# Kernel tuning notes

Measured on AMD Instinct MI355X. Metric: run time of the kernel, lower is better.

## Reference

```python
import jax, jax.numpy as jnp
import numpy as np

B, T, C = 4, 1024, 768
E, K = 8, 2               # n_exp, top_k
N = B * T                 # num_tokens
# eval-mode capacity: floor(K * eval_capacity(2.0) * N / E), rounded even, >= min_capacity(4)
CAP = 2048


def setup_inputs() -> dict:
    key = jax.random.key(0)
    k0, k1, k2, k3 = jax.random.split(key, 4)
    s = 0.02
    return {
        "x": jax.random.normal(k0, (B, T, C), jnp.float32),
        "w_g": jax.random.normal(k1, (E, C), jnp.float32) * s,
        "c_fc": jax.random.normal(k2, (E, C, 4 * C), jnp.float32) * s,
        "fc_bias": jnp.zeros((E, 1, 4 * C), jnp.float32),
        "c_proj": jax.random.normal(k3, (E, 4 * C, C), jnp.float32) * s,
        "proj_bias": jnp.zeros((E, 1, C), jnp.float32),
    }


def reference(x, w_g, c_fc, fc_bias, c_proj, proj_bias):
    xf = x.reshape(N, C)
    # ---- Router ----
    logits = xf @ w_g.T                                        # [N, E]
    top_v, top_i = jax.lax.top_k(logits, K)                    # [N, K]
    rows = jnp.arange(N)[:, None]
    masked = jnp.full((N, E), -jnp.inf, logits.dtype).at[rows, top_i].set(top_v)
    probs = jax.nn.softmax(masked, axis=-1)                    # [N, E] (zero off top-k)
    exp_mask = jax.nn.one_hot(top_i, E, dtype=jnp.float32)     # [N, K, E]
    exp_mask = exp_mask.transpose(1, 0, 2)                     # [K, N, E]
    # position of each assignment within its expert queue (top-1 assignments first)
    rank = jnp.cumsum(exp_mask.reshape(K * N, E), axis=0) - 1.0
    rank = rank.reshape(K, N, E)
    exp_mask = exp_mask * (rank < CAP)                         # drop over-capacity tokens
    rank_id = jnp.sum(exp_mask * rank, axis=-1).astype(jnp.int32)  # [K, N]
    exp_w = exp_mask * probs[None]                             # [K, N, E]
    rank_sc = jax.nn.one_hot(rank_id, CAP, dtype=jnp.float32)  # [K, N, CAP]
    cb_weight = jnp.einsum('kne,knc->nec', exp_w, rank_sc)     # [N, E, CAP] combine weights
    sec_mask = (cb_weight != 0).astype(xf.dtype)               # [N, E, CAP] dispatch mask
    # ---- Dispatch + batched experts (per-expert MLP via bmm) ----
    exp_in = jnp.einsum('nec,nd->ecd', sec_mask, xf)           # [E, CAP, C]
    h = jax.nn.gelu(jnp.einsum('ecd,edf->ecf', exp_in, c_fc) + fc_bias, approximate=False)
    exp_out = jnp.einsum('ecf,efd->ecd', h, c_proj) + proj_bias  # [E, CAP, C]
    # ---- Combine ----
    out = jnp.einsum('nec,ecd->nd', cb_weight, exp_out)        # [N, C]
    return out.reshape(B, T, C)
```

## Files before the change

### kernel.cpp

```cpp
#include <hip/hip_runtime.h>
#include <hip/hip_bf16.h>
#include <math.h>

#define N_TOK 4096
#define CDIM  768
#define E_EXP 8
#define CAPC  2048
#define HDIM  3072

typedef __attribute__((ext_vector_type(8))) short short8;
typedef __attribute__((ext_vector_type(4))) float floatx4;

#define VMCNT(n) asm volatile("s_waitcnt vmcnt(" #n ")" ::: "memory")
#define LGKM(n)  asm volatile("s_waitcnt lgkmcnt(" #n ")" ::: "memory")
#define SB0()    __builtin_amdgcn_sched_barrier(0)

static __device__ __forceinline__ unsigned short f2bf(float f) {
  __hip_bfloat16 h = __float2bfloat16(f);
  return __builtin_bit_cast(unsigned short, h);
}
static __device__ __forceinline__ float bf2f(unsigned short u) {
  return __builtin_bit_cast(float, (unsigned int)u << 16);
}

__global__ __launch_bounds__(256)
void prep_kernel(const float* __restrict__ cfc, const float* __restrict__ cpr,
                 __hip_bfloat16* __restrict__ wfcT, __hip_bfloat16* __restrict__ wprT,
                 const float* __restrict__ x, const float* __restrict__ wg,
                 int* __restrict__ eidx, float* __restrict__ pval)
{
  const int b = blockIdx.x;
  const int t = threadIdx.x;
  if (b < 4608) {
    const float* src;
    unsigned short* dstT;
    int Cc;
    if (b < 2304) {
      const int e = b / 288, rem = b % 288;
      const int kt = rem / 24, bx = rem % 24;
      src = cfc + (size_t)e * CDIM * HDIM + (size_t)(kt * 64) * HDIM + bx * 128;
      Cc = HDIM;
      dstT = (unsigned short*)wfcT + (((size_t)e * 24 + bx) * 12 + kt) * 8192;
    } else {
      const int bb = b - 2304;
      const int e = bb / 288, rem = bb % 288;
      const int kt = rem / 6, bx = rem % 6;
      src = cpr + (size_t)e * HDIM * CDIM + (size_t)(kt * 64) * CDIM + bx * 128;
      Cc = CDIM;
      dstT = (unsigned short*)wprT + (((size_t)e * 6 + bx) * 48 + kt) * 8192;
    }
    const int nq = t & 31, ko = t >> 5;
    const float* colp = src + (size_t)(ko * 8) * Cc + nq * 4;
    unsigned short obuf[4][8];
#pragma unroll
    for (int j = 0; j < 8; ++j) {
      const floatx4 v = __builtin_nontemporal_load((const floatx4*)(colp + (size_t)j * Cc));
      obuf[0][j] = f2bf(v[0]); obuf[1][j] = f2bf(v[1]);
      obuf[2][j] = f2bf(v[2]); obuf[3][j] = f2bf(v[3]);
    }
#pragma unroll
    for (int c = 0; c < 4; ++c)
      *(short8*)(dstT + (size_t)(nq * 4 + c) * 64 + ko * 8) = *(short8*)&obuf[c][0];
  } else {
    const int wv = t >> 6, lane = t & 63;
    const int n = (b - 4608) * 4 + wv;
    const float* xr = x + (size_t)n * CDIM;
    float acc[E_EXP] = {0.f, 0.f, 0.f, 0.f, 0.f, 0.f, 0.f, 0.f};
#pragma unroll
    for (int i = 0; i < CDIM / 64; ++i) {
      const float xv = xr[i * 64 + lane];
#pragma unroll
      for (int e = 0; e < E_EXP; ++e)
        acc[e] = fmaf(xv, wg[e * CDIM + i * 64 + lane], acc[e]);
    }
#pragma unroll
    for (int e = 0; e < E_EXP; ++e) {
#pragma unroll
      for (int off = 32; off > 0; off >>= 1)
        acc[e] += __shfl_xor(acc[e], off);
    }
    if (lane == 0) {
      int e0 = 0; float v0 = acc[0];
#pragma unroll
      for (int e = 1; e < E_EXP; ++e) if (acc[e] > v0) { v0 = acc[e]; e0 = e; }
      int e1 = -1; float v1 = -3.4e38f;
#pragma unroll
      for (int e = 0; e < E_EXP; ++e) if (e != e0 && acc[e] > v1) { v1 = acc[e]; e1 = e; }
      const float ex = __expf(v1 - v0);
      const float inv = 1.f / (1.f + ex);
      eidx[n] = e0; eidx[N_TOK + n] = e1;
      pval[n] = inv; pval[N_TOK + n] = ex * inv;
    }
  }
}

__global__ __launch_bounds__(256)
void scan_kernel(const int* __restrict__ eidx, int* __restrict__ slot,
                 int* __restrict__ slot_token, int* __restrict__ ecnt,
                 int* __restrict__ work2, int* __restrict__ wcnt)
{
  const int t = threadIdx.x;
  const int base = t * 32;
  int e_local[32];
  int cnt[E_EXP] = {0, 0, 0, 0, 0, 0, 0, 0};
#pragma unroll
  for (int i = 0; i < 32; ++i) {
    const int e = eidx[base + i];
    e_local[i] = e;
    cnt[e]++;
  }
  __shared__ int hist[256][E_EXP];
  __shared__ int secnt[E_EXP];
#pragma unroll
  for (int e = 0; e < E_EXP; ++e) hist[t][e] = cnt[e];
  __syncthreads();
  for (int off = 1; off < 256; off <<= 1) {
    int v[E_EXP] = {0, 0, 0, 0, 0, 0, 0, 0};
    if (t >= off) {
#pragma unroll
      for (int e = 0; e < E_EXP; ++e) v[e] = hist[t - off][e];
    }
    __syncthreads();
    if (t >= off) {
#pragma unroll
      for (int e = 0; e < E_EXP; ++e) hist[t][e] += v[e];
    }
    __syncthreads();
  }
  if (t == 255) {
#pragma unroll
    for (int e = 0; e < E_EXP; ++e) {
      const int tot = hist[255][e];
      const int c = tot < CAPC ? tot : CAPC;
      ecnt[e] = c;
      secnt[e] = c;
    }
  }
  __syncthreads();
  if (t == 0) {
    int n2 = 0;
    for (int e = 0; e < E_EXP; ++e) {
      const int c = secnt[e];
      const int t2 = (c + 127) >> 7;
      for (int b = 0; b < t2; ++b) work2[n2++] = (e << 8) | b;
    }
    wcnt[0] = n2 * 24;
    wcnt[1] = n2 * 6;
  }
  int run[E_EXP];
#pragma unroll
  for (int e = 0; e < E_EXP; ++e) run[e] = hist[t][e] - cnt[e];
#pragma unroll
  for (int i = 0; i < 32; ++i) {
    const int a = base + i;
    const int e = e_local[i];
    const int r = run[e]++;
    const int s = (r < CAPC) ? r : -1;
    slot[a] = s;
    if (s >= 0) slot_token[e * CAPC + s] = (a < N_TOK) ? a : (a - N_TOK);
  }
}

__global__ __launch_bounds__(256)
void dispatch_kernel(const float* __restrict__ x, const int* __restrict__ slot_token,
                     const int* __restrict__ ecnt, __hip_bfloat16* __restrict__ xin)
{
  const int wv = threadIdx.x >> 6, lane = threadIdx.x & 63;
  const int s = blockIdx.x * 4 + wv;
  const int e = s >> 11;
  if ((s & (CAPC - 1)) >= ecnt[e]) return;
  const int n = slot_token[s];
  unsigned short* orow = (unsigned short*)xin + (size_t)s * CDIM;
  const float4* xr = (const float4*)(x + (size_t)n * CDIM);
#pragma unroll
  for (int i = 0; i < 3; ++i) {
    const float4 v = xr[i * 64 + lane];
    ushort4 o;
    o.x = f2bf(v.x); o.y = f2bf(v.y); o.z = f2bf(v.z); o.w = f2bf(v.w);
    *(ushort4*)(orow + (size_t)(i * 64 + lane) * 4) = o;
  }
}

__device__ __forceinline__ void stage_a(const __hip_bfloat16* Ae, char* lds,
                                        int K, int kt, int wv, int lane)
{
  char* dst = lds + (kt & 1) * 32768;
#pragma unroll
  for (int j = 0; j < 4; ++j) {
    const int li = j * 32 + wv * 8 + (lane >> 3);
    const int kb = ((lane & 7) * 16) ^ ((li & 7) << 4);
    const char* g = (const char*)Ae + ((size_t)li * K + (size_t)kt * 64) * 2 + kb;
    __builtin_amdgcn_global_load_lds((const __attribute__((address_space(1))) unsigned int*)g,
                                     (__attribute__((address_space(3))) unsigned int*)(dst + j * 4096 + wv * 1024),
                                     16, 0, 0);
  }
}
__device__ __forceinline__ void stage_b(const char* BeT, char* lds,
                                        int kt, int wv, int lane)
{
  char* dst = lds + (kt & 1) * 32768 + 16384;
#pragma unroll
  for (int j = 0; j < 4; ++j) {
    const int li = j * 32 + wv * 8 + (lane >> 3);
    const int kb = ((lane & 7) * 16) ^ ((li & 7) << 4);
    const char* g = BeT + (size_t)kt * 16384 + li * 128 + kb;
    __builtin_amdgcn_global_load_lds((const __attribute__((address_space(1))) unsigned int*)g,
                                     (__attribute__((address_space(3))) unsigned int*)(dst + j * 4096 + wv * 1024),
                                     16, 0, 0);
  }
}

template<int VME, bool S2>
__device__ __forceinline__ void ktile2(int kt, char* lds,
                                       const __hip_bfloat16* Ae, const char* BeT,
                                       int K, floatx4 (&acc)[4][4],
                                       int wm, int wn, int fr, int fk, int wv, int lane)
{
  if constexpr (VME == 8) VMCNT(8); else VMCNT(0);
  __builtin_amdgcn_s_barrier();
  SB0();
  const char* bufA = lds + ((kt & 1) ? 32768 : 0);
  const char* bufB = bufA + 16384;
  short8 a[4][2], b[4][2];
#pragma unroll
  for (int mi = 0; mi < 4; ++mi) {
    const int lr = wm * 64 + mi * 16 + fr;
    a[mi][0] = *(const short8*)(bufA + lr * 128 + ((fk * 16) ^ ((lr & 7) << 4)));
  }
#pragma unroll
  for (int ni = 0; ni < 4; ++ni) {
    const int lj = wn * 64 + ni * 16 + fr;
    b[ni][0] = *(const short8*)(bufB + lj * 128 + ((fk * 16) ^ ((lj & 7) << 4)));
  }
  SB0();
#pragma unroll
  for (int mi = 0; mi < 4; ++mi) {
    const int lr = wm * 64 + mi * 16 + fr;
    a[mi][1] = *(const short8*)(bufA + lr * 128 + ((64 + fk * 16) ^ ((lr & 7) << 4)));
  }
#pragma unroll
  for (int ni = 0; ni < 4; ++ni) {
    const int lj = wn * 64 + ni * 16 + fr;
    b[ni][1] = *(const short8*)(bufB + lj * 128 + ((64 + fk * 16) ^ ((lj & 7) << 4)));
  }
  SB0();
  LGKM(8); SB0();
  __builtin_amdgcn_s_setprio(1);
#pragma unroll
  for (int mi = 0; mi < 4; ++mi)
#pragma unroll
    for (int ni = 0; ni < 4; ++ni)
      acc[mi][ni] = __builtin_amdgcn_mfma_f32_16x16x32_bf16(a[mi][0], b[ni][0], acc[mi][ni], 0, 0, 0);
  __builtin_amdgcn_s_setprio(0);
  SB0();
  LGKM(0); SB0();
  __builtin_amdgcn_s_setprio(1);
#pragma unroll
  for (int mi = 0; mi < 4; ++mi)
#pragma unroll
    for (int ni = 0; ni < 4; ++ni)
      acc[mi][ni] = __builtin_amdgcn_mfma_f32_16x16x32_bf16(a[mi][1], b[ni][1], acc[mi][ni], 0, 0, 0);
  __builtin_amdgcn_s_setprio(0);
  SB0();
  __builtin_amdgcn_s_barrier();
  if (S2) {
    stage_a(Ae, lds, K, kt + 2, wv, lane);
    stage_b(BeT, lds, kt + 2, wv, lane);
  }
  SB0();
}

static __device__ __forceinline__ float gelu_fast(float v) {
  const float u2 = v * (1.5957691216f + 0.0713548163f * v * v);
  const float ez = __expf(u2);
  return v * ez / (ez + 1.0f);
}

template<int EPI>
__device__ __forceinline__ void epilogue_bf16(floatx4 (&acc)[4][4], char* lds,
                                              const float* be, unsigned short* Cb,
                                              int Nn, int m0, int n0,
                                              int wm, int wn, int fr, int fk,
                                              int wv, int lane)
{
  unsigned short* ep = (unsigned short*)(lds + wv * 2048);
  float bcol[4];
#pragma unroll
  for (int ni = 0; ni < 4; ++ni) bcol[ni] = be[n0 + wn * 64 + ni * 16 + fr];
#pragma unroll
  for (int mi = 0; mi < 4; ++mi) {
#pragma unroll
    for (int ni = 0; ni < 4; ++ni)
#pragma unroll
      for (int j = 0; j < 4; ++j) {
        float v = acc[mi][ni][j] + bcol[ni];
        if (EPI == 1) v = gelu_fast(v);
        const int row = fk * 4 + j;
        *(unsigned short*)((char*)ep + row * 128 + ((ni * 32 + fr * 2) ^ (fk << 5))) = f2bf(v);
      }
    LGKM(0); SB0();
    const int r = lane & 15;
    const int grow = m0 + wm * 64 + mi * 16 + r;
#pragma unroll
    for (int it = 0; it < 2; ++it) {
      const int q = (lane >> 4) + it * 4;
      const short8 vv = *(const short8*)((char*)ep + r * 128 + ((q * 16) ^ ((r >> 2) << 5)));
      *(short8*)(Cb + (size_t)grow * Nn + n0 + wn * 64 + q * 8) = vv;
    }
    LGKM(0); SB0();
  }
}

__global__ __launch_bounds__(256, 2)
void gemm1p(const __hip_bfloat16* __restrict__ A, const __hip_bfloat16* __restrict__ Bt,
            const float* __restrict__ bias, __hip_bfloat16* __restrict__ Cout,
            const int* __restrict__ work, const int* __restrict__ wcnt)
{
  extern __shared__ __align__(16) char lds[];
  const int P = wcnt[0] / 24;
  const int x8 = blockIdx.x & 7, l = blockIdx.x >> 3;
  const int p0 = (x8 * P) >> 3;
  const int p1 = ((x8 + 1) * P) >> 3;
  const int px = p1 - p0;
  const int items_x = px * 24;

  const int t = threadIdx.x, wv = t >> 6, lane = t & 63;
  const int wm = wv >> 1, wn = wv & 1;
  const int fr = lane & 15, fk = lane >> 4;
  constexpr int ntk = CDIM / 64;

  for (int il = l; il < items_x; il += 64) {
    const int bx = il / px;
    const int p  = p0 + (il - bx * px);
    const int w = work[p];
    const int e = w >> 8, by = w & 255;

    const __hip_bfloat16* Ae = A + (size_t)e * CAPC * CDIM + (size_t)by * 128 * CDIM;
    const char* BeT = (const char*)Bt + (((size_t)e * 24 + bx) * 12) * 16384;

    floatx4 acc[4][4] = {};

    stage_a(Ae, lds, CDIM, 0, wv, lane);
    stage_b(BeT, lds, 0, wv, lane);
    stage_a(Ae, lds, CDIM, 1, wv, lane);
    stage_b(BeT, lds, 1, wv, lane);
    SB0();

#pragma unroll 1
    for (int kt = 0; kt < ntk - 2; ++kt)
      ktile2<8, true>(kt, lds, Ae, BeT, CDIM, acc, wm, wn, fr, fk, wv, lane);
    ktile2<8, false>(ntk - 2, lds, Ae, BeT, CDIM, acc, wm, wn, fr, fk, wv, lane);
    ktile2<0, false>(ntk - 1, lds, Ae, BeT, CDIM, acc, wm, wn, fr, fk, wv, lane);

    epilogue_bf16<1>(acc, lds,
                     bias + (size_t)e * HDIM,
                     (unsigned short*)Cout + (size_t)e * CAPC * HDIM,
                     HDIM, by * 128, bx * 128, wm, wn, fr, fk, wv, lane);
    __builtin_amdgcn_s_barrier();
    SB0();
  }
}

__global__ __launch_bounds__(256, 2)
void gemm2x(const __hip_bfloat16* __restrict__ A, const __hip_bfloat16* __restrict__ Bt,
            const float* __restrict__ bias, __hip_bfloat16* __restrict__ Cout,
            const int* __restrict__ work, const int* __restrict__ wcnt)
{
  extern __shared__ __align__(16) char lds[];
  const int T = wcnt[1];
  const int bId = blockIdx.x;
  const int cpx = (T + 7) >> 3;
  if ((bId >> 3) >= cpx) return;
  const int idx = (bId & 7) * cpx + (bId >> 3);
  if (idx >= T) return;
  const int p = idx / 6;
  const int bx0 = idx % 6;
  const int bx = (p & 1) ? (5 - bx0) : bx0;
  const int w = work[p];
  const int e = w >> 8, by = w & 255;

  const int t = threadIdx.x, wv = t >> 6, lane = t & 63;
  const int wm = wv >> 1, wn = wv & 1;
  const int fr = lane & 15, fk = lane >> 4;
  constexpr int ntk = HDIM / 64;

  const __hip_bfloat16* Ae = A + (size_t)e * CAPC * HDIM + (size_t)by * 128 * HDIM;
  const char* BeT = (const char*)Bt + (((size_t)e * 6 + bx) * 48) * 16384;

  floatx4 acc[4][4] = {};

  stage_a(Ae, lds, HDIM, 0, wv, lane);
  stage_b(BeT, lds, 0, wv, lane);
  stage_a(Ae, lds, HDIM, 1, wv, lane);
  stage_b(BeT, lds, 1, wv, lane);
  SB0();

#pragma unroll 1
  for (int kt = 0; kt < ntk - 2; ++kt)
    ktile2<8, true>(kt, lds, Ae, BeT, HDIM, acc, wm, wn, fr, fk, wv, lane);
  ktile2<8, false>(ntk - 2, lds, Ae, BeT, HDIM, acc, wm, wn, fr, fk, wv, lane);
  ktile2<0, false>(ntk - 1, lds, Ae, BeT, HDIM, acc, wm, wn, fr, fk, wv, lane);

  epilogue_bf16<2>(acc, lds,
                   bias + (size_t)e * CDIM,
                   (unsigned short*)Cout + (size_t)e * CAPC * CDIM,
                   CDIM, by * 128, bx * 128, wm, wn, fr, fk, wv, lane);
}

__global__ __launch_bounds__(256)
void combine_kernel(const __hip_bfloat16* __restrict__ eout, const int* __restrict__ eidx,
                    const float* __restrict__ pval, const int* __restrict__ slot,
                    float* __restrict__ out)
{
  const int wv = threadIdx.x >> 6, lane = threadIdx.x & 63;
  const int n = blockIdx.x * 4 + wv;
  const int e0 = eidx[n], e1 = eidx[N_TOK + n];
  int s0 = slot[n], s1 = slot[N_TOK + n];
  const float w0 = (s0 >= 0) ? pval[n] : 0.f;
  const float w1 = (s1 >= 0) ? pval[N_TOK + n] : 0.f;
  s0 = (s0 >= 0) ? s0 : 0;
  s1 = (s1 >= 0) ? s1 : 0;
  const ushort4* r0 = (const ushort4*)((const unsigned short*)eout + ((size_t)e0 * CAPC + s0) * CDIM);
  const ushort4* r1 = (const ushort4*)((const unsigned short*)eout + ((size_t)e1 * CAPC + s1) * CDIM);
  float4* o = (float4*)(out + (size_t)n * CDIM);
#pragma unroll
  for (int i = 0; i < 3; ++i) {
    const ushort4 a = r0[i * 64 + lane];
    const ushort4 b = r1[i * 64 + lane];
    float4 c;
    c.x = w0 * bf2f(a.x) + w1 * bf2f(b.x);
    c.y = w0 * bf2f(a.y) + w1 * bf2f(b.y);
    c.z = w0 * bf2f(a.z) + w1 * bf2f(b.z);
    c.w = w0 * bf2f(a.w) + w1 * bf2f(b.w);
    o[i * 64 + lane] = c;
  }
}

extern "C" void kernel_launch(void* const* d_in, const int* in_sizes, int n_in,
                              void* d_out, int out_size, void* d_ws, size_t ws_size,
                              hipStream_t stream)
{
  const float* x   = (const float*)d_in[0];
  const float* wg  = (const float*)d_in[1];
  const float* cfc = (const float*)d_in[2];
  const float* fcb = (const float*)d_in[3];
  const float* cpr = (const float*)d_in[4];
  const float* prb = (const float*)d_in[5];
  float* out = (float*)d_out;

  char* ws = (char*)d_ws;
  size_t off = 0;
  auto take = [&](size_t bytes) -> void* {
    void* p = ws + off;
    off += (bytes + 255) & ~(size_t)255;
    return p;
  };
  __hip_bfloat16* wfcT = (__hip_bfloat16*)take((size_t)E_EXP * HDIM * CDIM * 2);
  __hip_bfloat16* wprT = (__hip_bfloat16*)take((size_t)E_EXP * CDIM * HDIM * 2);
  __hip_bfloat16* xin  = (__hip_bfloat16*)take((size_t)E_EXP * CAPC * CDIM * 2);
  __hip_bfloat16* hbuf = (__hip_bfloat16*)take((size_t)E_EXP * CAPC * HDIM * 2);
  __hip_bfloat16* eout = (__hip_bfloat16*)take((size_t)E_EXP * CAPC * CDIM * 2);
  int*   eidx = (int*)take((size_t)2 * N_TOK * 4);
  float* pv   = (float*)take((size_t)2 * N_TOK * 4);
  int*   slot = (int*)take((size_t)2 * N_TOK * 4);
  int*   stok = (int*)take((size_t)E_EXP * CAPC * 4);
  int*   ecnt = (int*)take((size_t)E_EXP * 4);
  int*   work2 = (int*)take((size_t)128 * 4);
  int*   wcnt = (int*)take((size_t)2 * 4);

  hipFuncSetAttribute((const void*)gemm1p,
                      hipFuncAttributeMaxDynamicSharedMemorySize, 65536);
  hipFuncSetAttribute((const void*)gemm2x,
                      hipFuncAttributeMaxDynamicSharedMemorySize, 65536);

  prep_kernel<<<4608 + 1024, 256, 0, stream>>>(cfc, cpr, wfcT, wprT, x, wg, eidx, pv);
  scan_kernel<<<1, 256, 0, stream>>>(eidx, slot, stok, ecnt, work2, wcnt);
  dispatch_kernel<<<(E_EXP * CAPC) / 4, 256, 0, stream>>>(x, stok, ecnt, xin);

  gemm1p<<<512, 256, 65536, stream>>>(xin, wfcT, fcb, hbuf, work2, wcnt);
  gemm2x<<<768, 256, 65536, stream>>>(hbuf, wprT, prb, eout, work2, wcnt);

  combine_kernel<<<N_TOK / 4, 256, 0, stream>>>(eout, eidx, pv, slot, out);
}
```

Measured before the change: 168.7 us.

## Prefetch next work item's first k-tiles during gemm1 epilogue, cheaper GELU

The persistent gemm1 loop now issues the first two A/B k-tile loads for the next work item before running the current item's epilogue. The epilogue moves to a separate 8 KB LDS region past the 64 KB staging area so the prefetch does not clash with it. This hides the pipeline fill latency behind the GELU and store epilogue. In exchange the kernel needs 72 KB of dynamic LDS, which may lower occupancy from 2 blocks per CU. GELU also switches to exp2f with pre-scaled constants and a hardware reciprocal in place of a divide.

```diff
diff --git a/kernel.cpp b/kernel.cpp
--- a/kernel.cpp
+++ b/kernel.cpp
@@ -271,19 +271,19 @@
 }
 
 static __device__ __forceinline__ float gelu_fast(float v) {
-  const float u2 = v * (1.5957691216f + 0.0713548163f * v * v);
-  const float ez = __expf(u2);
-  return v * ez / (ez + 1.0f);
+  const float u2 = v * (2.3022184f + 0.1029434f * v * v);
+  const float ez = exp2f(u2);
+  return v * ez * __builtin_amdgcn_rcpf(ez + 1.0f);
 }
 
 template<int EPI>
-__device__ __forceinline__ void epilogue_bf16(floatx4 (&acc)[4][4], char* lds,
+__device__ __forceinline__ void epilogue_bf16(floatx4 (&acc)[4][4], char* epb,
                                               const float* be, unsigned short* Cb,
                                               int Nn, int m0, int n0,
                                               int wm, int wn, int fr, int fk,
                                               int wv, int lane)
 {
-  unsigned short* ep = (unsigned short*)(lds + wv * 2048);
+  unsigned short* ep = (unsigned short*)(epb + wv * 2048);
   float bcol[4];
 #pragma unroll
   for (int ni = 0; ni < 4; ++ni) bcol[ni] = be[n0 + wn * 64 + ni * 16 + fr];
@@ -329,22 +329,24 @@
   const int fr = lane & 15, fk = lane >> 4;
   constexpr int ntk = CDIM / 64;
 
-  for (int il = l; il < items_x; il += 64) {
-    const int bx = il / px;
-    const int p  = p0 + (il - bx * px);
-    const int w = work[p];
-    const int e = w >> 8, by = w & 255;
-
-    const __hip_bfloat16* Ae = A + (size_t)e * CAPC * CDIM + (size_t)by * 128 * CDIM;
-    const char* BeT = (const char*)Bt + (((size_t)e * 24 + bx) * 12) * 16384;
-
+  int il = l;
+  if (il >= items_x) return;
+
+  int bx = il / px;
+  int p  = p0 + (il - bx * px);
+  int w  = work[p];
+  int e  = w >> 8, by = w & 255;
+  const __hip_bfloat16* Ae = A + (size_t)e * CAPC * CDIM + (size_t)by * 128 * CDIM;
+  const char* BeT = (const char*)Bt + (((size_t)e * 24 + bx) * 12) * 16384;
+
+  stage_a(Ae, lds, CDIM, 0, wv, lane);
+  stage_b(BeT, lds, 0, wv, lane);
+  stage_a(Ae, lds, CDIM, 1, wv, lane);
+  stage_b(BeT, lds, 1, wv, lane);
+  SB0();
+
+  for (; il < items_x; il += 64) {
     floatx4 acc[4][4] = {};
-
-    stage_a(Ae, lds, CDIM, 0, wv, lane);
-    stage_b(BeT, lds, 0, wv, lane);
-    stage_a(Ae, lds, CDIM, 1, wv, lane);
-    stage_b(BeT, lds, 1, wv, lane);
-    SB0();
 
 #pragma unroll 1
     for (int kt = 0; kt < ntk - 2; ++kt)
@@ -352,12 +354,31 @@
     ktile2<8, false>(ntk - 2, lds, Ae, BeT, CDIM, acc, wm, wn, fr, fk, wv, lane);
     ktile2<0, false>(ntk - 1, lds, Ae, BeT, CDIM, acc, wm, wn, fr, fk, wv, lane);
 
-    epilogue_bf16<1>(acc, lds,
+    const int il2 = il + 64;
+    const __hip_bfloat16* Ae2 = Ae; const char* BeT2 = BeT;
+    int e2 = e, by2 = by, bx2 = bx;
+    if (il2 < items_x) {
+      bx2 = il2 / px;
+      const int p2 = p0 + (il2 - bx2 * px);
+      const int w2 = work[p2];
+      e2 = w2 >> 8; by2 = w2 & 255;
+      Ae2 = A + (size_t)e2 * CAPC * CDIM + (size_t)by2 * 128 * CDIM;
+      BeT2 = (const char*)Bt + (((size_t)e2 * 24 + bx2) * 12) * 16384;
+      stage_a(Ae2, lds, CDIM, 0, wv, lane);
+      stage_b(BeT2, lds, 0, wv, lane);
+      stage_a(Ae2, lds, CDIM, 1, wv, lane);
+      stage_b(BeT2, lds, 1, wv, lane);
+      SB0();
+    }
+
+    epilogue_bf16<1>(acc, lds + 65536,
                      bias + (size_t)e * HDIM,
                      (unsigned short*)Cout + (size_t)e * CAPC * HDIM,
                      HDIM, by * 128, bx * 128, wm, wn, fr, fk, wv, lane);
     __builtin_amdgcn_s_barrier();
     SB0();
+
+    Ae = Ae2; BeT = BeT2; e = e2; by = by2; bx = bx2;
   }
 }
 
@@ -469,7 +490,7 @@
   int*   wcnt = (int*)take((size_t)2 * 4);
 
   hipFuncSetAttribute((const void*)gemm1p,
-                      hipFuncAttributeMaxDynamicSharedMemorySize, 65536);
+                      hipFuncAttributeMaxDynamicSharedMemorySize, 73728);
   hipFuncSetAttribute((const void*)gemm2x,
                       hipFuncAttributeMaxDynamicSharedMemorySize, 65536);
 
@@ -477,7 +498,7 @@
   scan_kernel<<<1, 256, 0, stream>>>(eidx, slot, stok, ecnt, work2, wcnt);
   dispatch_kernel<<<(E_EXP * CAPC) / 4, 256, 0, stream>>>(x, stok, ecnt, xin);
 
-  gemm1p<<<512, 256, 65536, stream>>>(xin, wfcT, fcb, hbuf, work2, wcnt);
+  gemm1p<<<512, 256, 73728, stream>>>(xin, wfcT, fcb, hbuf, work2, wcnt);
   gemm2x<<<768, 256, 65536, stream>>>(hbuf, wprT, prb, eout, work2, wcnt);
 
   combine_kernel<<<N_TOK / 4, 256, 0, stream>>>(eout, eidx, pv, slot, out);
```

After: 166.0 us. No clear change (-1.6%).
